# Kernel tuning notes

Measured on AMD Instinct MI355X. Metric: run time of the kernel, lower is better.

The kernel has to match this reference:

```python
import jax, jax.numpy as jnp
import numpy as np

N = 50000
NEG_SLOPE = 0.2


def add_self_loops(edge_index, n):
    loops = jnp.arange(n, dtype=edge_index.dtype)
    return jnp.concatenate([edge_index, jnp.stack([loops, loops])], axis=1)


def gat_layer(x, edge_index, W, a_src, a_dst, b, heads, ch):
    # x: [N, F_in], W: [F_in, heads*ch], a_src/a_dst: [heads, ch], b: [heads*ch]
    n = x.shape[0]
    src, dst = edge_index[0], edge_index[1]
    h = (x @ W).reshape(n, heads, ch)                      # [N, H, C]
    alpha_src = jnp.sum(h * a_src, axis=-1)                # [N, H]
    alpha_dst = jnp.sum(h * a_dst, axis=-1)                # [N, H]
    e = jax.nn.leaky_relu(alpha_src[src] + alpha_dst[dst], NEG_SLOPE)  # [E, H]
    # segment softmax over incoming edges of each destination node
    m = jax.ops.segment_max(e, dst, num_segments=n)        # [N, H]
    ex = jnp.exp(e - m[dst])                               # [E, H]
    denom = jax.ops.segment_sum(ex, dst, num_segments=n)   # [N, H]
    alpha = ex / (denom[dst] + 1e-16)                      # [E, H]
    msg = h[src] * alpha[:, :, None]                       # [E, H, C]
    out = jax.ops.segment_sum(msg, dst, num_segments=n)    # [N, H, C]
    return out.reshape(n, heads * ch) + b


def setup_inputs() -> dict:
    key = jax.random.key(0)
    ks = jax.random.split(key, 12)
    input_dim, hidden_dim, output_dim, heads = 128, 32, 64, 4
    E = 1600000
    x = jax.random.normal(ks[0], (N, input_dim), dtype=jnp.float32)
    edge_index = jax.random.randint(ks[1], (2, E), 0, N, dtype=jnp.int64)
    s1 = 1.0 / np.sqrt(input_dim)
    s2 = 1.0 / np.sqrt(hidden_dim * heads)
    W1 = jax.random.uniform(ks[2], (input_dim, heads * hidden_dim), jnp.float32, -s1, s1)
    a_src1 = jax.random.uniform(ks[3], (heads, hidden_dim), jnp.float32, -s1, s1)
    a_dst1 = jax.random.uniform(ks[4], (heads, hidden_dim), jnp.float32, -s1, s1)
    b1 = jnp.zeros((heads * hidden_dim,), jnp.float32)
    W2 = jax.random.uniform(ks[5], (heads * hidden_dim, output_dim), jnp.float32, -s2, s2)
    a_src2 = jax.random.uniform(ks[6], (1, output_dim), jnp.float32, -s2, s2)
    a_dst2 = jax.random.uniform(ks[7], (1, output_dim), jnp.float32, -s2, s2)
    b2 = jnp.zeros((output_dim,), jnp.float32)
    return {"x": x, "edge_index": edge_index,
            "W1": W1, "a_src1": a_src1, "a_dst1": a_dst1, "b1": b1,
            "W2": W2, "a_src2": a_src2, "a_dst2": a_dst2, "b2": b2}


def reference(x, edge_index, W1, a_src1, a_dst1, b1, W2, a_src2, a_dst2, b2):
    n = x.shape[0]
    ei = add_self_loops(edge_index, n)
    h = gat_layer(x, ei, W1, a_src1, a_dst1, b1, heads=4, ch=32)
    h = jax.nn.relu(h)
    out = gat_layer(h, ei, W2, a_src2, a_dst2, b2, heads=1, ch=64)
    return out
```

## Files before the change

### kernel.cpp

```cpp
#include <hip/hip_runtime.h>
#include <hip/hip_bf16.h>
#include <hip/hip_fp16.h>


#define LRELU_SLOPE 0.2f
#define NBMAX 200
#define NBLK  512
#define BCAP  16384
#define CAPIMG 16384

typedef _Float16 f16x8 __attribute__((ext_vector_type(8)));
typedef _Float16 f16x4 __attribute__((ext_vector_type(4)));
typedef float f32x4 __attribute__((ext_vector_type(4)));


__global__ __launch_bounds__(256) void k1_kernel(
    const int* __restrict__ ei_src, const int* __restrict__ ei_dst,
    unsigned int* __restrict__ records, int* __restrict__ gfill,
    const float* __restrict__ X, const float* __restrict__ W1,
    __half* __restrict__ h1h,
    const float* __restrict__ a_src1, const float* __restrict__ a_dst1,
    float* __restrict__ asrc1, float* __restrict__ adst1,
    const float* __restrict__ W2,
    const float* __restrict__ a_src2, const float* __restrict__ a_dst2,
    float* __restrict__ wa2,
    int E, int chunk, int N, int G1B, int ALB) {
    __shared__ __align__(16) char smem[34816];
    int t = threadIdx.x;
    int bid = blockIdx.x;

    if (bid < NBLK) {
        int* cnt  = (int*)smem;
        int* base = ((int*)smem) + NBMAX;
        for (int i = t; i < NBMAX; i += 256) cnt[i] = 0;
        __syncthreads();
        int begin = bid * chunk;
        int endE = min(E, begin + chunk);
        for (int e = begin + t; e < endE; e += 256) atomicAdd(&cnt[ei_dst[e] >> 8], 1);
        __syncthreads();
        for (int i = t; i < NBMAX; i += 256) {
            int c = cnt[i];
            base[i] = c ? atomicAdd(&gfill[i], c) : 0;
            cnt[i] = 0;
        }
        __syncthreads();
        for (int e = begin + t; e < endE; e += 256) {
            int s = ei_src[e], d = ei_dst[e];
            int bkt = d >> 8;
            unsigned int rec = (unsigned int)d | ((unsigned int)s << 16);
            int r = atomicAdd(&cnt[bkt], 1);
            records[(size_t)bkt * BCAP + base[bkt] + r] = rec;
        }
        return;
    }

    if (bid < NBLK + G1B) {
        constexpr int KP = 136;
        _Float16* wlds = (_Float16*)smem;
        int gb = bid - NBLK;
        int wv = t >> 6, lane = t & 63;
        int quad = lane >> 4, m16 = lane & 15;
        for (int i = t; i < 4096; i += 256) {
            int k = i >> 5;
            int n0 = (i & 31) << 2;
            float4 v = *(const float4*)(W1 + k * 128 + n0);
            wlds[(n0 + 0) * KP + k] = (_Float16)v.x;
            wlds[(n0 + 1) * KP + k] = (_Float16)v.y;
            wlds[(n0 + 2) * KP + k] = (_Float16)v.z;
            wlds[(n0 + 3) * KP + k] = (_Float16)v.w;
        }
        __syncthreads();

        int row = gb * 64 + wv * 16 + m16;
        int rowC = min(row, N - 1);
        const float* xp = X + (size_t)rowC * 128;

        f32x4 acc[8];
#pragma unroll
        for (int nt = 0; nt < 8; ++nt) acc[nt] = (f32x4)0.f;

        for (int kt = 0; kt < 128; kt += 32) {
            float4 v0 = *(const float4*)(xp + kt + quad * 8);
            float4 v1 = *(const float4*)(xp + kt + quad * 8 + 4);
            f16x8 af;
            af[0] = (_Float16)v0.x; af[1] = (_Float16)v0.y;
            af[2] = (_Float16)v0.z; af[3] = (_Float16)v0.w;
            af[4] = (_Float16)v1.x; af[5] = (_Float16)v1.y;
            af[6] = (_Float16)v1.z; af[7] = (_Float16)v1.w;
#pragma unroll
            for (int nt = 0; nt < 8; ++nt) {
                f16x8 bf = *(const f16x8*)(&wlds[(nt * 16 + m16) * KP + kt + quad * 8]);
                acc[nt] = __builtin_amdgcn_mfma_f32_16x16x32_f16(af, bf, acc[nt], 0, 0, 0);
            }
        }

        int rowBaseW = gb * 64 + wv * 16;
#pragma unroll
        for (int r = 0; r < 4; ++r) {
            int orow = rowBaseW + quad * 4 + r;
            if (orow < N) {
#pragma unroll
                for (int nt = 0; nt < 8; ++nt)
                    h1h[(size_t)orow * 128 + nt * 16 + m16] = __float2half(acc[nt][r]);
            }
        }
        return;
    }

    int aid = bid - NBLK - G1B;
    if (aid < ALB) {
        float* waL = (float*)smem;
        {
            int k = t >> 1, grp = t & 1;
            const float* wrow = W1 + k * 128;
            const float* abase = grp ? a_dst1 : a_src1;
#pragma unroll
            for (int h = 0; h < 4; ++h) {
                const float* av = abase + h * 32;
                const float* wr = wrow + h * 32;
                float acc = 0.f;
                for (int c = 0; c < 32; ++c) acc += wr[c] * av[c];
                waL[(grp * 4 + h) * 128 + k] = acc;
            }
        }
        __syncthreads();
        int row = aid * 256 + t;
        if (row < N) {
            const float4* x4 = (const float4*)(X + (size_t)row * 128);
            float p[8];
#pragma unroll
            for (int o = 0; o < 8; ++o) p[o] = 0.f;
            for (int k4 = 0; k4 < 32; ++k4) {
                float4 xv = x4[k4];
#pragma unroll
                for (int o = 0; o < 8; ++o) {
                    float4 wv = ((const float4*)(waL + o * 128))[k4];
                    p[o] += xv.x * wv.x + xv.y * wv.y + xv.z * wv.z + xv.w * wv.w;
                }
            }
            float4 ps = {p[0], p[1], p[2], p[3]};
            float4 pd = {p[4], p[5], p[6], p[7]};
            ((float4*)asrc1)[row] = ps;
            ((float4*)adst1)[row] = pd;
        }
        return;
    }

    if (t < 128) {
        const float* wr = W2 + t * 64;
        float acc = 0.f;
        for (int c = 0; c < 64; ++c) acc += wr[c] * a_src2[c];
        wa2[t] = acc;
    } else {
        int k = t - 128;
        const float* wr = W2 + k * 64;
        float acc = 0.f;
        for (int c = 0; c < 64; ++c) acc += wr[c] * a_dst2[c];
        wa2[128 + k] = acc;
    }
}


__global__ __launch_bounds__(256) void scan_blocksums_kernel(const int* __restrict__ gfill,
                                                             int* __restrict__ bsums,
                                                             int* __restrict__ row_ptr,
                                                             int nblocks, int n, int total) {
    __shared__ int buf[2][256];
    int t = threadIdx.x;
    int v0 = 0;
    if (t < nblocks) v0 = gfill[t] + min(256, n - (t << 8));
    buf[0][t] = v0;
    __syncthreads();
    int pi = 0;
#pragma unroll
    for (int off = 1; off < 256; off <<= 1) {
        int v = buf[pi][t];
        if (t >= off) v += buf[pi][t - off];
        buf[pi ^ 1][t] = v;
        __syncthreads();
        pi ^= 1;
    }
    if (t < nblocks) bsums[t] = (t == 0) ? 0 : buf[pi][t - 1];
    if (t == 0) row_ptr[n] = total;
}

__global__ __launch_bounds__(256) void csr_fused_kernel(const unsigned int* __restrict__ records,
                                                        const int* __restrict__ gfill,
                                                        const int* __restrict__ bsums,
                                                        int* __restrict__ row_ptr,
                                                        unsigned short* __restrict__ col,
                                                        int N) {
    __shared__ unsigned short img[CAPIMG];
    __shared__ int cnt[2][256];
    __shared__ int lfill[256];
    int t = threadIdx.x, b = blockIdx.x;
    int bBase = b << 8;
    int bEnd = min(bBase + 256, N);
    int rbase = bsums[b];
    int c = gfill[b];
    int size = c + (bEnd - bBase);
    bool lds = (size <= CAPIMG);
    const unsigned int* r = records + (size_t)b * BCAP;
    int gi = bBase + t;
    cnt[0][t] = (gi < bEnd) ? 1 : 0;
    __syncthreads();
    for (int i = t; i < c; i += 256) atomicAdd(&cnt[0][r[i] & 255], 1);
    __syncthreads();
    int d = cnt[0][t];
    int pi = 0;
#pragma unroll
    for (int off = 1; off < 256; off <<= 1) {
        int v = cnt[pi][t];
        if (t >= off) v += cnt[pi][t - off];
        cnt[pi ^ 1][t] = v;
        __syncthreads();
        pi ^= 1;
    }
    int local = cnt[pi][t] - d;
    if (gi < bEnd) {
        row_ptr[gi] = rbase + local;
        lfill[t] = local + 1;
        if (lds) img[local] = (unsigned short)gi;
        else col[rbase + local] = (unsigned short)gi;
    }
    __syncthreads();
    for (int i = t; i < c; i += 256) {
        unsigned int rec = r[i];
        int d8 = rec & 255;
        unsigned short s = (unsigned short)(rec >> 16);
        int p = atomicAdd(&lfill[d8], 1);
        if (lds) img[p] = s;
        else col[rbase + p] = s;
    }
    __syncthreads();
    if (lds) {
        for (int i = t; i < size; i += 256) col[rbase + i] = img[i];
    }
}


__global__ __launch_bounds__(256) void gemm2_mfma_kernel(const __half* __restrict__ Xh,
                                                         const float* __restrict__ W,
                                                         __half* __restrict__ outh, int nrows) {
    constexpr int KP = 136;
    __shared__ _Float16 wlds[64 * KP];
    int t = threadIdx.x;
    int wv = t >> 6, lane = t & 63;
    int quad = lane >> 4, m16 = lane & 15;
    for (int i = t; i < 2048; i += 256) {
        int k = i >> 4;
        int n0 = (i & 15) << 2;
        float4 v = *(const float4*)(W + k * 64 + n0);
        wlds[(n0 + 0) * KP + k] = (_Float16)v.x;
        wlds[(n0 + 1) * KP + k] = (_Float16)v.y;
        wlds[(n0 + 2) * KP + k] = (_Float16)v.z;
        wlds[(n0 + 3) * KP + k] = (_Float16)v.w;
    }
    __syncthreads();

    int row = blockIdx.x * 64 + wv * 16 + m16;
    int rowC = min(row, nrows - 1);
    const _Float16* xp = (const _Float16*)Xh + (size_t)rowC * 128;

    f32x4 acc[4];
#pragma unroll
    for (int nt = 0; nt < 4; ++nt) acc[nt] = (f32x4)0.f;

    for (int kt = 0; kt < 128; kt += 32) {
        f16x8 af = *(const f16x8*)(xp + kt + quad * 8);
#pragma unroll
        for (int nt = 0; nt < 4; ++nt) {
            f16x8 bf = *(const f16x8*)(&wlds[(nt * 16 + m16) * KP + kt + quad * 8]);
            acc[nt] = __builtin_amdgcn_mfma_f32_16x16x32_f16(af, bf, acc[nt], 0, 0, 0);
        }
    }

    int rowBaseW = blockIdx.x * 64 + wv * 16;
#pragma unroll
    for (int r = 0; r < 4; ++r) {
        int orow = rowBaseW + quad * 4 + r;
        if (orow < nrows) {
#pragma unroll
            for (int nt = 0; nt < 4; ++nt)
                outh[(size_t)orow * 64 + nt * 16 + m16] = __float2half(acc[nt][r]);
        }
    }
}


__global__ __launch_bounds__(256) void agg1_kernel(const __half* __restrict__ h1h,
                                                   const float* __restrict__ asrc,
                                                   const float* __restrict__ adst,
                                                   const int* __restrict__ row_ptr,
                                                   const unsigned short* __restrict__ col,
                                                   const float* __restrict__ b1,
                                                   const float* __restrict__ wa2,
                                                   __half* __restrict__ out,
                                                   float* __restrict__ asrc2,
                                                   float* __restrict__ adst2, int n) {
    int wave = threadIdx.x >> 6;
    int lane = threadIdx.x & 63;
    int node = blockIdx.x * 4 + wave;
    if (node >= n) return;
    int half = lane >> 5;
    int m = lane & 31;
    int head = m >> 3;
    const char* __restrict__ h1c = (const char*)h1h;
    const char* __restrict__ asc = (const char*)asrc;
    unsigned moff = (unsigned)m << 3;
    unsigned aoff = (unsigned)head << 2;
    float ad = adst[node * 4 + head];
    int start = row_ptr[node], end = row_ptr[node + 1];
    float a0c = 0.f, a1c = 0.f, a2c = 0.f, a3c = 0.f, s = 0.f;
    for (int base = start; base < end; base += 64) {
        int cnt = min(64, end - base);
        int idx = base + lane;
        int myS = (idx < end) ? (int)col[idx] : 0;
        for (int j = 0; j < cnt; j += 12) {
            int jj[6];
            int sv[6];
#pragma unroll
            for (int k = 0; k < 6; ++k) {
                jj[k] = j + 2 * k + half;
                sv[k] = __shfl(myS, jj[k], 64);
            }
            f16x4 v[6];
            float as[6];
#pragma unroll
            for (int k = 0; k < 6; ++k) {
                v[k]  = *(const f16x4*)(h1c + ((((unsigned)sv[k]) << 8) | moff));
                as[k] = *(const float*)(asc + ((((unsigned)sv[k]) << 4) | aoff));
            }
#pragma unroll
            for (int k = 0; k < 6; ++k) {
                float e = as[k] + ad;
                e = fmaxf(e, LRELU_SLOPE * e);
                float p = (jj[k] < cnt) ? __expf(e) : 0.f;
                a0c = fmaf(p, (float)v[k][0], a0c);
                a1c = fmaf(p, (float)v[k][1], a1c);
                a2c = fmaf(p, (float)v[k][2], a2c);
                a3c = fmaf(p, (float)v[k][3], a3c);
                s += p;
            }
        }
    }
    a0c += __shfl_xor(a0c, 32, 64);
    a1c += __shfl_xor(a1c, 32, 64);
    a2c += __shfl_xor(a2c, 32, 64);
    a3c += __shfl_xor(a3c, 32, 64);
    s   += __shfl_xor(s, 32, 64);
    float ps = 0.f, pd = 0.f;
    if (half == 0) {
        float inv = 1.f / (s + 1e-16f);
        float4 bb = ((const float4*)b1)[m];
        float o0 = fmaxf(fmaf(a0c, inv, bb.x), 0.f);
        float o1 = fmaxf(fmaf(a1c, inv, bb.y), 0.f);
        float o2 = fmaxf(fmaf(a2c, inv, bb.z), 0.f);
        float o3 = fmaxf(fmaf(a3c, inv, bb.w), 0.f);
        f16x4 o;
        o[0] = (_Float16)o0; o[1] = (_Float16)o1;
        o[2] = (_Float16)o2; o[3] = (_Float16)o3;
        ((f16x4*)out)[node * 32 + m] = o;
        float4 w2s = ((const float4*)wa2)[m];
        float4 w2d = ((const float4*)(wa2 + 128))[m];
        ps = o0 * w2s.x + o1 * w2s.y + o2 * w2s.z + o3 * w2s.w;
        pd = o0 * w2d.x + o1 * w2d.y + o2 * w2d.z + o3 * w2d.w;
    }
#pragma unroll
    for (int o = 1; o <= 16; o <<= 1) {
        ps += __shfl_xor(ps, o, 64);
        pd += __shfl_xor(pd, o, 64);
    }
    if (lane == 0) {
        asrc2[node] = ps;
        adst2[node] = pd;
    }
}

__global__ __launch_bounds__(256) void agg2_kernel(const __half* __restrict__ h2bh,
                                                   const float* __restrict__ asrc,
                                                   const float* __restrict__ adst,
                                                   const int* __restrict__ row_ptr,
                                                   const unsigned short* __restrict__ col,
                                                   const float* __restrict__ b2,
                                                   float* __restrict__ out, int n) {
    int wave = threadIdx.x >> 6;
    int lane = threadIdx.x & 63;
    int node = blockIdx.x * 4 + wave;
    if (node >= n) return;
    int eslot = lane >> 3;
    int sub = lane & 7;
    const char* __restrict__ h2c = (const char*)h2bh;
    unsigned coff = (unsigned)sub << 4;
    float ad = adst[node];
    int start = row_ptr[node], end = row_ptr[node + 1];
    float acc[8];
#pragma unroll
    for (int c = 0; c < 8; ++c) acc[c] = 0.f;
    float s = 0.f;
    for (int base = start; base < end; base += 16) {
        int iA = base + eslot;
        int iB = iA + 8;
        int sA = (int)col[min(iA, end - 1)];
        int sB = (int)col[min(iB, end - 1)];
        f16x8 vA = *(const f16x8*)(h2c + ((((unsigned)sA) << 7) | coff));
        f16x8 vB = *(const f16x8*)(h2c + ((((unsigned)sB) << 7) | coff));
        float eA = asrc[sA] + ad;
        float eB = asrc[sB] + ad;
        eA = fmaxf(eA, LRELU_SLOPE * eA);
        eB = fmaxf(eB, LRELU_SLOPE * eB);
        float pA = (iA < end) ? __expf(eA) : 0.f;
        float pB = (iB < end) ? __expf(eB) : 0.f;
#pragma unroll
        for (int c = 0; c < 8; ++c) acc[c] = fmaf(pA, (float)vA[c], acc[c]);
#pragma unroll
        for (int c = 0; c < 8; ++c) acc[c] = fmaf(pB, (float)vB[c], acc[c]);
        s += pA + pB;
    }
#pragma unroll
    for (int o = 8; o < 64; o <<= 1) {
#pragma unroll
        for (int c = 0; c < 8; ++c) acc[c] += __shfl_xor(acc[c], o, 64);
        s += __shfl_xor(s, o, 64);
    }
    if (lane < 8) {
        float inv = 1.f / (s + 1e-16f);
        float4 bb0 = ((const float4*)b2)[sub * 2];
        float4 bb1 = ((const float4*)b2)[sub * 2 + 1];
        float4 o0, o1;
        o0.x = fmaf(acc[0], inv, bb0.x);
        o0.y = fmaf(acc[1], inv, bb0.y);
        o0.z = fmaf(acc[2], inv, bb0.z);
        o0.w = fmaf(acc[3], inv, bb0.w);
        o1.x = fmaf(acc[4], inv, bb1.x);
        o1.y = fmaf(acc[5], inv, bb1.y);
        o1.z = fmaf(acc[6], inv, bb1.z);
        o1.w = fmaf(acc[7], inv, bb1.w);
        ((float4*)(out + (size_t)node * 64))[sub * 2] = o0;
        ((float4*)(out + (size_t)node * 64))[sub * 2 + 1] = o1;
    }
}


extern "C" void kernel_launch(void* const* d_in, const int* in_sizes, int n_in,
                              void* d_out, int out_size, void* d_ws, size_t ws_size,
                              hipStream_t stream) {
    const float* x      = (const float*)d_in[0];
    const int*   ei     = (const int*)d_in[1];
    const float* W1     = (const float*)d_in[2];
    const float* a_src1 = (const float*)d_in[3];
    const float* a_dst1 = (const float*)d_in[4];
    const float* b1     = (const float*)d_in[5];
    const float* W2     = (const float*)d_in[6];
    const float* a_src2 = (const float*)d_in[7];
    const float* a_dst2 = (const float*)d_in[8];
    const float* b2     = (const float*)d_in[9];
    float* out = (float*)d_out;

    const int N = in_sizes[0] / 128;
    const int E = in_sizes[1] / 2;
    const int total = E + N;
    const int nBuckets = (N + 255) >> 8;

    char* ws = (char*)d_ws;
    size_t off = 0;
    auto alloc = [&](size_t bytes) {
        void* p = ws + off;
        off += (bytes + 255) & ~(size_t)255;
        return p;
    };
    float* regionA = (float*)alloc((size_t)N * 128 * 4);
    __half* h1h   = (__half*)alloc((size_t)N * 128 * 2);
    __half* h2bh  = (__half*)alloc((size_t)N * 64 * 2);
    float* asrc1  = (float*)alloc((size_t)N * 4 * 4);
    float* adst1  = (float*)alloc((size_t)N * 4 * 4);
    float* asrc2  = (float*)alloc((size_t)N * 4);
    float* adst2  = (float*)alloc((size_t)N * 4);
    int*   row_ptr= (int*)alloc((size_t)(N + 1) * 4);
    int*   gfill  = (int*)alloc((size_t)nBuckets * 4);
    int*   bsums  = (int*)alloc((size_t)nBuckets * 4);
    float* wa2    = (float*)alloc(256 * 4);
    unsigned short* col = (unsigned short*)alloc((size_t)total * 2);

    unsigned int* records = (unsigned int*)regionA;
    __half* h2in = (__half*)regionA;
    (void)ws_size; (void)n_in; (void)out_size;

    const int* ei_src = ei;
    const int* ei_dst = ei + E;

    const int chunk = (E + NBLK - 1) / NBLK;
    const int G1B = (N + 63) / 64;
    const int ALB = (N + 255) / 256;

    hipMemsetAsync(gfill, 0, (size_t)nBuckets * 4, stream);

    k1_kernel<<<NBLK + G1B + ALB + 1, 256, 0, stream>>>(
        ei_src, ei_dst, records, gfill,
        x, W1, h1h, a_src1, a_dst1, asrc1, adst1,
        W2, a_src2, a_dst2, wa2,
        E, chunk, N, G1B, ALB);

    scan_blocksums_kernel<<<1, 256, 0, stream>>>(gfill, bsums, row_ptr, nBuckets, N, total);
    csr_fused_kernel<<<nBuckets, 256, 0, stream>>>(records, gfill, bsums, row_ptr, col, N);

    agg1_kernel<<<(N + 3) / 4, 256, 0, stream>>>(h1h, asrc1, adst1,
                                                 row_ptr, col, b1, wa2,
                                                 h2in, asrc2, adst2, N);

    gemm2_mfma_kernel<<<(N + 63) / 64, 256, 0, stream>>>(h2in, W2, h2bh, N);
    agg2_kernel<<<(N + 3) / 4, 256, 0, stream>>>(h2bh, asrc2, adst2,
                                                 row_ptr, col, b2, out, N);
}
```

Before: 242.2 us.

## Stage edge records in LDS and sort by bucket before coalesced scatter; fold blocksum scan into CSR kernel

The edge-partitioning blocks now load each chunk once into shared memory, build a per-bucket histogram, prefix-scan it, and locally sort the records by bucket before writing them out in contiguous runs. This replaces the second global read of the edge arrays and the scattered per-edge global writes. The separate single-block scan kernel is removed, and each CSR block computes its own base offset with a wavefront reduction over gfill. The trade is more LDS use and barriers per block, and it relies on the chunk size fitting within SCAP.

```diff
diff --git a/kernel.cpp b/kernel.cpp
--- a/kernel.cpp
+++ b/kernel.cpp
@@ -8,6 +8,7 @@
 #define NBLK  512
 #define BCAP  16384
 #define CAPIMG 16384
+#define SCAP  3328
 
 typedef _Float16 f16x8 __attribute__((ext_vector_type(8)));
 typedef _Float16 f16x4 __attribute__((ext_vector_type(4)));
@@ -30,26 +31,54 @@
     int bid = blockIdx.x;
 
     if (bid < NBLK) {
-        int* cnt  = (int*)smem;
-        int* base = ((int*)smem) + NBMAX;
-        for (int i = t; i < NBMAX; i += 256) cnt[i] = 0;
+        int* hist   = (int*)smem;
+        int* base_g = hist + 256;
+        int* cur    = base_g + 256;
+        int* sbuf   = cur + 256;
+        unsigned int* ustage = (unsigned int*)(sbuf + 512);
+        unsigned int* sstage = ustage + SCAP;
+
+        hist[t] = 0;
         __syncthreads();
         int begin = bid * chunk;
         int endE = min(E, begin + chunk);
-        for (int e = begin + t; e < endE; e += 256) atomicAdd(&cnt[ei_dst[e] >> 8], 1);
-        __syncthreads();
-        for (int i = t; i < NBMAX; i += 256) {
-            int c = cnt[i];
-            base[i] = c ? atomicAdd(&gfill[i], c) : 0;
-            cnt[i] = 0;
-        }
-        __syncthreads();
-        for (int e = begin + t; e < endE; e += 256) {
-            int s = ei_src[e], d = ei_dst[e];
-            int bkt = d >> 8;
+        int nE = endE - begin;
+        for (int i = t; i < nE; i += 256) {
+            int s = ei_src[begin + i], d = ei_dst[begin + i];
             unsigned int rec = (unsigned int)d | ((unsigned int)s << 16);
-            int r = atomicAdd(&cnt[bkt], 1);
-            records[(size_t)bkt * BCAP + base[bkt] + r] = rec;
+            ustage[i] = rec;
+            atomicAdd(&hist[d >> 8], 1);
+        }
+        __syncthreads();
+        int h = hist[t];
+        if (t < NBMAX && h) base_g[t] = atomicAdd(&gfill[t], h);
+        sbuf[t] = h;
+        __syncthreads();
+        int pi = 0;
+#pragma unroll
+        for (int off = 1; off < 256; off <<= 1) {
+            int v = sbuf[pi * 256 + t];
+            if (t >= off) v += sbuf[pi * 256 + t - off];
+            sbuf[(pi ^ 1) * 256 + t] = v;
+            __syncthreads();
+            pi ^= 1;
+        }
+        int excl = sbuf[pi * 256 + t] - h;
+        hist[t] = excl;
+        cur[t] = excl;
+        __syncthreads();
+        for (int i = t; i < nE; i += 256) {
+            unsigned int rec = ustage[i];
+            int bkt = (rec & 0xFFFF) >> 8;
+            int r = atomicAdd(&cur[bkt], 1);
+            sstage[r] = rec;
+        }
+        __syncthreads();
+        for (int i = t; i < nE; i += 256) {
+            unsigned int rec = sstage[i];
+            int bkt = (rec & 0xFFFF) >> 8;
+            int g = base_g[bkt] + (i - hist[bkt]);
+            records[(size_t)bkt * BCAP + g] = rec;
         }
         return;
     }
@@ -161,49 +190,31 @@
 }
 
 
-__global__ __launch_bounds__(256) void scan_blocksums_kernel(const int* __restrict__ gfill,
-                                                             int* __restrict__ bsums,
-                                                             int* __restrict__ row_ptr,
-                                                             int nblocks, int n, int total) {
-    __shared__ int buf[2][256];
-    int t = threadIdx.x;
-    int v0 = 0;
-    if (t < nblocks) v0 = gfill[t] + min(256, n - (t << 8));
-    buf[0][t] = v0;
-    __syncthreads();
-    int pi = 0;
-#pragma unroll
-    for (int off = 1; off < 256; off <<= 1) {
-        int v = buf[pi][t];
-        if (t >= off) v += buf[pi][t - off];
-        buf[pi ^ 1][t] = v;
-        __syncthreads();
-        pi ^= 1;
-    }
-    if (t < nblocks) bsums[t] = (t == 0) ? 0 : buf[pi][t - 1];
-    if (t == 0) row_ptr[n] = total;
-}
-
 __global__ __launch_bounds__(256) void csr_fused_kernel(const unsigned int* __restrict__ records,
                                                         const int* __restrict__ gfill,
-                                                        const int* __restrict__ bsums,
                                                         int* __restrict__ row_ptr,
                                                         unsigned short* __restrict__ col,
-                                                        int N) {
+                                                        int N, int total) {
     __shared__ unsigned short img[CAPIMG];
     __shared__ int cnt[2][256];
     __shared__ int lfill[256];
+    __shared__ int rbuf[4];
     int t = threadIdx.x, b = blockIdx.x;
     int bBase = b << 8;
     int bEnd = min(bBase + 256, N);
-    int rbase = bsums[b];
+    int pv = (t < b) ? gfill[t] : 0;
+#pragma unroll
+    for (int o = 1; o < 64; o <<= 1) pv += __shfl_xor(pv, o, 64);
+    if ((t & 63) == 0) rbuf[t >> 6] = pv;
     int c = gfill[b];
+    int gi = bBase + t;
+    cnt[0][t] = (gi < bEnd) ? 1 : 0;
+    if (b == 0 && t == 0) row_ptr[N] = total;
+    __syncthreads();
+    int rbase = rbuf[0] + rbuf[1] + rbuf[2] + rbuf[3] + (b << 8);
     int size = c + (bEnd - bBase);
     bool lds = (size <= CAPIMG);
     const unsigned int* r = records + (size_t)b * BCAP;
-    int gi = bBase + t;
-    cnt[0][t] = (gi < bEnd) ? 1 : 0;
-    __syncthreads();
     for (int i = t; i < c; i += 256) atomicAdd(&cnt[0][r[i] & 255], 1);
     __syncthreads();
     int d = cnt[0][t];
@@ -478,7 +489,6 @@
     float* adst2  = (float*)alloc((size_t)N * 4);
     int*   row_ptr= (int*)alloc((size_t)(N + 1) * 4);
     int*   gfill  = (int*)alloc((size_t)nBuckets * 4);
-    int*   bsums  = (int*)alloc((size_t)nBuckets * 4);
     float* wa2    = (float*)alloc(256 * 4);
     unsigned short* col = (unsigned short*)alloc((size_t)total * 2);
 
@@ -501,8 +511,7 @@
         W2, a_src2, a_dst2, wa2,
         E, chunk, N, G1B, ALB);
 
-    scan_blocksums_kernel<<<1, 256, 0, stream>>>(gfill, bsums, row_ptr, nBuckets, N, total);
-    csr_fused_kernel<<<nBuckets, 256, 0, stream>>>(records, gfill, bsums, row_ptr, col, N);
+    csr_fused_kernel<<<nBuckets, 256, 0, stream>>>(records, gfill, row_ptr, col, N, total);
 
     agg1_kernel<<<(N + 3) / 4, 256, 0, stream>>>(h1h, asrc1, adst1,
                                                  row_ptr, col, b1, wa2,
```

Measured after the change: 240.0 us. About the same (-0.9%).
